# Kernel optimization log

Hardware: AMD Instinct MI355X
Metric: run time of the kernel (lower is better)

Reference implementation:

```python
import jax, jax.numpy as jnp
import numpy as np

Q_HEADS, KV_HEADS, DIMS = 16, 4, 1024
HEAD_DIM = DIMS // Q_HEADS          # 64
GROUPS = Q_HEADS // KV_HEADS        # 4


def rope(x):
    # x: [..., s, d]; base-10 thetas, positions start at 1 (per source RoPE)
    s, d = x.shape[-2], x.shape[-1]
    thetas = 10.0 ** (-jnp.arange(d // 2, dtype=jnp.float32))
    angles = jnp.arange(1, s + 1, dtype=jnp.float32)[:, None] * thetas  # [s, d/2]
    cos, sin = jnp.cos(angles), jnp.sin(angles)
    xr, xi = x[..., ::2], x[..., 1::2]
    outr = xr * cos - xi * sin
    outi = xr * sin + xi * cos
    return jnp.stack([outr, outi], axis=-1).reshape(x.shape)  # re-interleave


def setup_inputs() -> dict:
    key = jax.random.key(0)
    ks = jax.random.split(key, 5)
    b, s, in_dim = 4, 2048, 1024
    q = jax.random.normal(ks[0], (b, s, in_dim), dtype=jnp.float32)
    mask = jnp.tril(jnp.ones((s, s), dtype=jnp.float32))  # 1 = keep, 0 = masked
    sc = 1.0 / np.sqrt(in_dim)
    Wq = jax.random.normal(ks[1], (in_dim, Q_HEADS, HEAD_DIM), dtype=jnp.float32) * sc
    Wk = jax.random.normal(ks[2], (in_dim, KV_HEADS, HEAD_DIM), dtype=jnp.float32) * sc
    Wv = jax.random.normal(ks[3], (in_dim, KV_HEADS, HEAD_DIM), dtype=jnp.float32) * sc
    Wo = jax.random.normal(ks[4], (KV_HEADS * HEAD_DIM, in_dim), dtype=jnp.float32) * (1.0 / np.sqrt(KV_HEADS * HEAD_DIM))
    return {"q": q, "mask": mask, "Wq": Wq, "Wk": Wk, "Wv": Wv, "Wo": Wo}


def reference(q, mask, Wq, Wk, Wv, Wo):
    b, s, in_dim = q.shape
    # projections (DenseGeneral, no bias)
    qh = jnp.einsum('bsi,ihd->bshd', q, Wq)   # [b, s, 16, 64]
    kh = jnp.einsum('bsi,ihd->bshd', q, Wk)   # [b, s, 4, 64]  (kv = q)
    vh = jnp.einsum('bsi,ihd->bshd', q, Wv)
    # '... s (h g) d -> ... g h s d' with g=GROUPS
    qh = qh.reshape(b, s, KV_HEADS, GROUPS, HEAD_DIM).transpose(0, 3, 2, 1, 4)  # [b,g,h,s,d]
    kh = kh.transpose(0, 2, 1, 3)  # [b, h, s, d]
    vh = vh.transpose(0, 2, 1, 3)
    qh = rope(qh)
    kh = rope(kh)
    # NOTE: source einsum sums over group axis g
    scores = jnp.einsum('bghsd,bhad->bhsa', qh, kh)  # [b, h, s, s]
    scores = scores - (1.0 / mask - 1.0)             # mask==0 -> -inf
    attn = jax.nn.softmax(scores / jnp.float32(HEAD_DIM ** 0.5), axis=-1)
    out = jnp.einsum('bhsa,bhad->bhsd', attn, vh)    # [b, h, s, d]
    out = out.transpose(0, 2, 1, 3).reshape(b, s, KV_HEADS * HEAD_DIM)
    return out @ Wo  # [b, s, in_dim]
```

## Files before the change

### kernel.cpp

```cpp
#include <hip/hip_runtime.h>
#include <math.h>

#define BATCH 4
#define SEQ   2048
#define DIN   1024
#define KVH   4
#define HD    64
#define MTOT  (BATCH*SEQ)
#define NPROJ 768
#define PROJ_STRIDE (BATCH*KVH*SEQ*HD)
#define NCHUNK_TOT 80

typedef unsigned short ushort_t;
typedef __attribute__((ext_vector_type(8))) short short8;
typedef __attribute__((ext_vector_type(4))) float f32x4;

#define QSCALE (0.125f * 1.44269504088896340736f)

__device__ inline ushort_t f2bf(float x) {
    union { float f; unsigned int u; } v; v.f = x;
    unsigned int r = v.u + 0x7fffu + ((v.u >> 16) & 1u);
    return (ushort_t)(r >> 16);
}
__device__ inline ushort_t f2bf_trunc(float x) {
    return (ushort_t)(__float_as_uint(x) >> 16);
}

__device__ inline void load16_lds(const ushort_t* g, ushort_t* l) {
    __builtin_amdgcn_global_load_lds(
        (const __attribute__((address_space(1))) void*)g,
        (__attribute__((address_space(3))) void*)l, 16, 0, 0);
}

__global__ __launch_bounds__(256) void prep_kernel(
        const float* __restrict__ Wq, const float* __restrict__ Wk,
        const float* __restrict__ Wv, const float* __restrict__ Wo,
        const float* __restrict__ X,
        ushort_t* __restrict__ Wcat_t, ushort_t* __restrict__ Wo_t,
        float2* __restrict__ ctab, ushort_t* __restrict__ Y) {
    const int bx = blockIdx.x;
    const int tid = threadIdx.x;
    if (bx < 4096) {
        int idx = bx * 256 + tid;
        if (idx < NPROJ * DIN) {
            int n = idx >> 10, k = idx & 1023;
            float v;
            if (n < 256) {
                const float* p = Wq + (size_t)k * 1024 + (n >> 6) * 256 + (n & 63);
                v = p[0] + p[64] + p[128] + p[192];
            } else if (n < 512) {
                v = Wk[(size_t)k * 256 + (n - 256)];
            } else {
                v = Wv[(size_t)k * 256 + (n - 512)];
            }
            Wcat_t[idx] = f2bf(v);
        } else {
            int t = idx - NPROJ * DIN;
            int n = t >> 8, k = t & 255;
            Wo_t[t] = f2bf(Wo[(size_t)k * 1024 + n]);
        }
    } else if (bx < 4352) {
        int t = (bx - 4096) * 256 + tid;
        int j = t & 31, s = t >> 5;
        float ang = (float)(s + 1) * exp10f(-(float)j);
        float sn, cs;
        sincosf(ang, &sn, &cs);
        ctab[t] = make_float2(cs, sn);
    } else {
        int i = ((bx - 4352) * 256 + tid) * 4;
        float4 v = *(const float4*)&X[i];
        ushort4 o;
        o.x = f2bf(v.x); o.y = f2bf(v.y); o.z = f2bf(v.z); o.w = f2bf(v.w);
        *(ushort4*)&Y[i] = o;
    }
}

template<int OUT_MODE>
__global__ __launch_bounds__(256) void gemm_mfma_kernel(
        const ushort_t* __restrict__ A, const ushort_t* __restrict__ Bt,
        float* __restrict__ Y, ushort_t* __restrict__ Qbf,
        ushort_t* __restrict__ Kbf, ushort_t* __restrict__ Vt,
        const float2* __restrict__ ctab, int K, int N) {
    __shared__ __align__(16) ushort_t As[128 * 64];
    __shared__ __align__(16) ushort_t Bs[64 * 64];
    const int tid  = threadIdx.x;
    const int w    = tid >> 6, lane = tid & 63;
    const int m15  = lane & 15, quad = lane >> 4;
    const int wm   = (w >> 1) * 64, wn = (w & 1) * 32;
    const int m0   = blockIdx.y * 128, n0 = blockIdx.x * 64;
    const int r8   = lane >> 3;
    const int cs   = (((lane & 7) + r8) & 7) * 8;
    const int rotr = (m15 & 7) * 8;
    const int off0 = (quad * 8 + 64 - rotr) & 63;
    const int off1 = (32 + quad * 8 + 64 - rotr) & 63;

    f32x4 acc[4][2];
    #pragma unroll
    for (int i = 0; i < 4; ++i)
        #pragma unroll
        for (int j = 0; j < 2; ++j) acc[i][j] = (f32x4){0.f, 0.f, 0.f, 0.f};

    for (int k0 = 0; k0 < K; k0 += 64) {
        __syncthreads();
        #pragma unroll
        for (int p = 0; p < 4; ++p)
            load16_lds(A + (size_t)(m0 + w * 32 + p * 8 + r8) * K + k0 + cs,
                       As + (w * 32 + p * 8) * 64);
        #pragma unroll
        for (int p = 0; p < 2; ++p)
            load16_lds(Bt + (size_t)(n0 + w * 16 + p * 8 + r8) * K + k0 + cs,
                       Bs + (w * 16 + p * 8) * 64);
        __syncthreads();

        short8 af[4][2], bfm[2][2];
        #pragma unroll
        for (int i = 0; i < 4; ++i) {
            af[i][0] = *(const short8*)&As[(wm + i * 16 + m15) * 64 + off0];
            af[i][1] = *(const short8*)&As[(wm + i * 16 + m15) * 64 + off1];
        }
        #pragma unroll
        for (int j = 0; j < 2; ++j) {
            bfm[j][0] = *(const short8*)&Bs[(wn + j * 16 + m15) * 64 + off0];
            bfm[j][1] = *(const short8*)&Bs[(wn + j * 16 + m15) * 64 + off1];
        }
        #pragma unroll
        for (int i = 0; i < 4; ++i)
            #pragma unroll
            for (int j = 0; j < 2; ++j) {
                acc[i][j] = __builtin_amdgcn_mfma_f32_16x16x32_bf16(
                                af[i][0], bfm[j][0], acc[i][j], 0, 0, 0);
                acc[i][j] = __builtin_amdgcn_mfma_f32_16x16x32_bf16(
                                af[i][1], bfm[j][1], acc[i][j], 0, 0, 0);
            }
    }

    if (OUT_MODE == 0) {
        #pragma unroll
        for (int i = 0; i < 4; ++i)
            #pragma unroll
            for (int r = 0; r < 4; ++r) {
                size_t row = (size_t)(m0 + wm + i * 16 + quad * 4 + r);
                #pragma unroll
                for (int j = 0; j < 2; ++j)
                    Y[row * N + n0 + wn + j * 16 + m15] = acc[i][j][r];
            }
    } else {
        #pragma unroll
        for (int j = 0; j < 2; ++j) {
            int c = n0 + wn + j * 16 + m15;
            int proj = c >> 8, cc = c & 255;
            int hd = cc >> 6, d = cc & 63;
            if (proj < 2) {
                int jj = d >> 1;
                float sgn = (d & 1) ? 1.0f : -1.0f;
                float qs  = (proj == 0) ? QSCALE : 1.0f;
                ushort_t* dst = (proj ? Kbf : Qbf) + (size_t)hd * SEQ * HD + d;
                #pragma unroll
                for (int i = 0; i < 4; ++i)
                    #pragma unroll
                    for (int r = 0; r < 4; ++r) {
                        int m = m0 + wm + i * 16 + quad * 4 + r;
                        int b = m >> 11, s = m & (SEQ - 1);
                        float x = acc[i][j][r];
                        float p = __shfl_xor(x, 1);
                        float2 ct = ctab[s * 32 + jj];
                        float o = (x * ct.x + sgn * p * ct.y) * qs;
                        dst[(((size_t)b * KVH) * SEQ + s) * HD] = f2bf(o);
                    }
            } else {
                ushort_t* Vp = Vt + (((size_t)hd * HD) + d) * SEQ;
                #pragma unroll
                for (int i = 0; i < 4; ++i)
                    #pragma unroll
                    for (int r = 0; r < 4; ++r) {
                        int m = m0 + wm + i * 16 + quad * 4 + r;
                        int b = m >> 11, s = m & (SEQ - 1);
                        Vp[(size_t)b * KVH * HD * SEQ + s] = f2bf(acc[i][j][r]);
                    }
            }
        }
    }
}

__global__ __launch_bounds__(256) void attn_mfma_kernel(
        const ushort_t* __restrict__ Qbf, const ushort_t* __restrict__ Kbf,
        const ushort_t* __restrict__ Vtbf, float* __restrict__ pO,
        float* __restrict__ pL) {
    __shared__ __align__(16) ushort_t Ks[64][72];
    __shared__ __align__(16) ushort_t Vts[64][72];
    __shared__ __align__(16) ushort_t Ps[4][16][72];
    const int tid  = threadIdx.x;
    const int w    = tid >> 6, lane = tid & 63;
    const int m15  = lane & 15, quad = lane >> 4;
    const int bh   = blockIdx.y;
    const int f    = 79 - blockIdx.x;
    int qt, ch;
    if (f < 8)       { qt = f;                    ch = 0; }
    else if (f < 24) { qt = 8  + ((f - 8) >> 1);  ch = (f - 8) & 1; }
    else if (f < 48) { qt = 16 + (f - 24) / 3;    ch = (f - 24) % 3; }
    else             { qt = 24 + ((f - 48) >> 2); ch = (f - 48) & 3; }
    const int q0 = qt * 64;
    const int kt_beg = ch * 8;
    const int kt_end = min(kt_beg + 8, qt + 1);

    const ushort_t* Qb  = Qbf  + (size_t)bh * SEQ * HD;
    const ushort_t* Kb  = Kbf  + (size_t)bh * SEQ * HD;
    const ushort_t* Vtb = Vtbf + (size_t)bh * HD * SEQ;

    const int qrow = q0 + w * 16 + m15;
    short8 qf0 = *(const short8*)(Qb + (size_t)qrow * HD + quad * 8);
    short8 qf1 = *(const short8*)(Qb + (size_t)qrow * HD + 32 + quad * 8);

    f32x4 o[4];
    #pragma unroll
    for (int nt = 0; nt < 4; ++nt) o[nt] = (f32x4){0.f, 0.f, 0.f, 0.f};
    float lacc[4] = {0.f, 0.f, 0.f, 0.f};

    const int sc_ = tid & 7;
    const int sr_ = tid >> 3;

    short8 pk0, pk1, pv0, pv1;
    {
        const int k0 = kt_beg * 64;
        pk0 = *(const short8*)(Kb  + (size_t)(k0 + sr_) * HD + sc_ * 8);
        pk1 = *(const short8*)(Kb  + (size_t)(k0 + sr_ + 32) * HD + sc_ * 8);
        pv0 = *(const short8*)(Vtb + (size_t)sr_ * SEQ + k0 + sc_ * 8);
        pv1 = *(const short8*)(Vtb + (size_t)(sr_ + 32) * SEQ + k0 + sc_ * 8);
    }

    for (int kt = kt_beg; kt < kt_end; ++kt) {
        const int k0 = kt * 64;
        __syncthreads();
        *(short8*)&Ks[sr_][sc_*8]       = pk0;
        *(short8*)&Ks[sr_ + 32][sc_*8]  = pk1;
        *(short8*)&Vts[sr_][sc_*8]      = pv0;
        *(short8*)&Vts[sr_ + 32][sc_*8] = pv1;
        __syncthreads();

        if (kt + 1 < kt_end) {
            const int kn = k0 + 64;
            pk0 = *(const short8*)(Kb  + (size_t)(kn + sr_) * HD + sc_ * 8);
            pk1 = *(const short8*)(Kb  + (size_t)(kn + sr_ + 32) * HD + sc_ * 8);
            pv0 = *(const short8*)(Vtb + (size_t)sr_ * SEQ + kn + sc_ * 8);
            pv1 = *(const short8*)(Vtb + (size_t)(sr_ + 32) * SEQ + kn + sc_ * 8);
        }

        f32x4 sc4[4];
        #pragma unroll
        for (int nt = 0; nt < 4; ++nt) {
            f32x4 c = {0.f, 0.f, 0.f, 0.f};
            c = __builtin_amdgcn_mfma_f32_16x16x32_bf16(
                    qf0, *(const short8*)&Ks[nt*16 + m15][quad*8], c, 0, 0, 0);
            c = __builtin_amdgcn_mfma_f32_16x16x32_bf16(
                    qf1, *(const short8*)&Ks[nt*16 + m15][32 + quad*8], c, 0, 0, 0);
            sc4[nt] = c;
        }
        if (kt == qt) {
            #pragma unroll
            for (int nt = 0; nt < 4; ++nt) {
                int colg = k0 + nt*16 + m15;
                #pragma unroll
                for (int r = 0; r < 4; ++r) {
                    int rowg = q0 + w*16 + quad*4 + r;
                    if (colg > rowg) sc4[nt][r] = -INFINITY;
                }
            }
        }

        #pragma unroll
        for (int nt = 0; nt < 4; ++nt)
            #pragma unroll
            for (int r = 0; r < 4; ++r) {
                float e = exp2f(sc4[nt][r]);
                lacc[r] += e;
                Ps[w][quad*4 + r][nt*16 + m15] = f2bf_trunc(e);
            }

        short8 pa0 = *(const short8*)&Ps[w][m15][quad*8];
        short8 pa1 = *(const short8*)&Ps[w][m15][32 + quad*8];
        #pragma unroll
        for (int nt = 0; nt < 4; ++nt) {
            o[nt] = __builtin_amdgcn_mfma_f32_16x16x32_bf16(
                        pa0, *(const short8*)&Vts[nt*16 + m15][quad*8], o[nt], 0, 0, 0);
            o[nt] = __builtin_amdgcn_mfma_f32_16x16x32_bf16(
                        pa1, *(const short8*)&Vts[nt*16 + m15][32 + quad*8], o[nt], 0, 0, 0);
        }
    }

    const int blk = bh * NCHUNK_TOT + f;
    #pragma unroll
    for (int r = 0; r < 4; ++r) {
        float ls = lacc[r];
        ls += __shfl_xor(ls, 1);
        ls += __shfl_xor(ls, 2);
        ls += __shfl_xor(ls, 4);
        ls += __shfl_xor(ls, 8);
        int row = w * 16 + quad * 4 + r;
        if (m15 == 0) pL[(size_t)blk * 64 + row] = ls;
        #pragma unroll
        for (int nt = 0; nt < 4; ++nt)
            pO[(size_t)blk * 4096 + row * 64 + nt * 16 + m15] = o[nt][r];
    }
}

__device__ inline int flat_of(int qt, int ch) {
    if (qt < 8)  return qt;
    if (qt < 16) return 8 + (qt - 8) * 2 + ch;
    if (qt < 24) return 24 + (qt - 16) * 3 + ch;
    return 48 + (qt - 24) * 4 + ch;
}

__global__ __launch_bounds__(256) void combine_kernel(
        const float* __restrict__ pO, const float* __restrict__ pL,
        ushort_t* __restrict__ Out) {
    const int qt = blockIdx.x, bh = blockIdx.y;
    const int tid = threadIdx.x;
    const int row = tid >> 2;
    const int cb = (tid & 3) * 16;
    const int nch = (qt >> 3) + 1;
    float acc[16] = {};
    float lsum = 0.f;
    for (int c = 0; c < nch; ++c) {
        int blk = bh * NCHUNK_TOT + flat_of(qt, c);
        const float* po = pO + (size_t)blk * 4096 + row * 64 + cb;
        lsum += pL[(size_t)blk * 64 + row];
        #pragma unroll
        for (int j = 0; j < 4; ++j) {
            float4 v = *(const float4*)&po[j * 4];
            acc[j*4+0] += v.x; acc[j*4+1] += v.y;
            acc[j*4+2] += v.z; acc[j*4+3] += v.w;
        }
    }
    float inv = 1.0f / lsum;
    int b = bh >> 2, h = bh & 3;
    int s = qt * 64 + row;
    ushort_t tmp[16];
    #pragma unroll
    for (int j = 0; j < 16; ++j) tmp[j] = f2bf(acc[j] * inv);
    ushort_t* dst = Out + ((size_t)b * SEQ + s) * (KVH * HD) + h * HD + cb;
    *(uint4*)dst = ((uint4*)tmp)[0];
    *(uint4*)(dst + 8) = ((uint4*)tmp)[1];
}

extern "C" void kernel_launch(void* const* d_in, const int* in_sizes, int n_in,
                              void* d_out, int out_size, void* d_ws, size_t ws_size,
                              hipStream_t stream) {
    const float* q  = (const float*)d_in[0];
    const float* Wq = (const float*)d_in[2];
    const float* Wk = (const float*)d_in[3];
    const float* Wv = (const float*)d_in[4];
    const float* Wo = (const float*)d_in[5];
    float* out = (float*)d_out;

    char* base = (char*)d_ws;
    ushort_t* wcat_t  = (ushort_t*)(base);
    ushort_t* wo_t    = (ushort_t*)(base + 0x180000);
    float2*   ctab    = (float2*)(base + 0x200000);
    ushort_t* qin_bf  = (ushort_t*)(base + 0x280000);
    ushort_t* attn_bf = (ushort_t*)(base + 0x280000);
    float*    pO      = (float*)(base + 0x680000);
    float*    pL      = (float*)(base + 0x1A80000);
    ushort_t* q_bf    = (ushort_t*)(base + 0x1B00000);
    ushort_t* k_bf    = (ushort_t*)(base + 0x1F00000);
    ushort_t* vt_bf   = (ushort_t*)(base + 0x2300000);

    prep_kernel<<<12544, 256, 0, stream>>>(Wq, Wk, Wv, Wo, q,
                                           wcat_t, wo_t, ctab, qin_bf);

    dim3 gproj(NPROJ / 64, MTOT / 128);
    gemm_mfma_kernel<1><<<gproj, 256, 0, stream>>>(
        qin_bf, wcat_t, nullptr, q_bf, k_bf, vt_bf, ctab, DIN, NPROJ);

    dim3 gattn(NCHUNK_TOT, BATCH * KVH);
    attn_mfma_kernel<<<gattn, 256, 0, stream>>>(q_bf, k_bf, vt_bf, pO, pL);

    dim3 gcomb(SEQ / 64, BATCH * KVH);
    combine_kernel<<<gcomb, 256, 0, stream>>>(pO, pL, attn_bf);

    dim3 gout(DIN / 64, MTOT / 128);
    gemm_mfma_kernel<0><<<gout, 256, 0, stream>>>(
        attn_bf, wo_t, out, nullptr, nullptr, nullptr, nullptr, KVH * HD, DIN);
}
```

Baseline: 178.2 us.

## Register-prefetch next GEMM K tile and stagger K start per block row

Result: no change. 178.3 us (+0.0%).

```diff
diff --git a/kernel.cpp b/kernel.cpp
--- a/kernel.cpp
+++ b/kernel.cpp
@@ -24,12 +24,6 @@
 }
 __device__ inline ushort_t f2bf_trunc(float x) {
     return (ushort_t)(__float_as_uint(x) >> 16);
-}
-
-__device__ inline void load16_lds(const ushort_t* g, ushort_t* l) {
-    __builtin_amdgcn_global_load_lds(
-        (const __attribute__((address_space(1))) void*)g,
-        (__attribute__((address_space(3))) void*)l, 16, 0, 0);
 }
 
 __global__ __launch_bounds__(256) void prep_kernel(
@@ -89,28 +83,51 @@
     const int wm   = (w >> 1) * 64, wn = (w & 1) * 32;
     const int m0   = blockIdx.y * 128, n0 = blockIdx.x * 64;
     const int r8   = lane >> 3;
+    const int c8   = (lane & 7) * 8;
     const int cs   = (((lane & 7) + r8) & 7) * 8;
     const int rotr = (m15 & 7) * 8;
     const int off0 = (quad * 8 + 64 - rotr) & 63;
     const int off1 = (32 + quad * 8 + 64 - rotr) & 63;
 
+    const int niter = K >> 6;
+    const int kst   = blockIdx.y & (niter - 1);
+
     f32x4 acc[4][2];
     #pragma unroll
     for (int i = 0; i < 4; ++i)
         #pragma unroll
         for (int j = 0; j < 2; ++j) acc[i][j] = (f32x4){0.f, 0.f, 0.f, 0.f};
 
-    for (int k0 = 0; k0 < K; k0 += 64) {
+    short8 ra[4], rb[2];
+    {
+        const int k0 = kst * 64;
+        #pragma unroll
+        for (int p = 0; p < 4; ++p)
+            ra[p] = *(const short8*)(A + (size_t)(m0 + w * 32 + p * 8 + r8) * K + k0 + cs);
+        #pragma unroll
+        for (int p = 0; p < 2; ++p)
+            rb[p] = *(const short8*)(Bt + (size_t)(n0 + w * 16 + p * 8 + r8) * K + k0 + cs);
+    }
+
+    for (int it = 0; it < niter; ++it) {
         __syncthreads();
         #pragma unroll
         for (int p = 0; p < 4; ++p)
-            load16_lds(A + (size_t)(m0 + w * 32 + p * 8 + r8) * K + k0 + cs,
-                       As + (w * 32 + p * 8) * 64);
+            *(short8*)&As[(w * 32 + p * 8 + r8) * 64 + c8] = ra[p];
         #pragma unroll
         for (int p = 0; p < 2; ++p)
-            load16_lds(Bt + (size_t)(n0 + w * 16 + p * 8 + r8) * K + k0 + cs,
-                       Bs + (w * 16 + p * 8) * 64);
+            *(short8*)&Bs[(w * 16 + p * 8 + r8) * 64 + c8] = rb[p];
         __syncthreads();
+
+        if (it + 1 < niter) {
+            const int kn = ((kst + it + 1) & (niter - 1)) * 64;
+            #pragma unroll
+            for (int p = 0; p < 4; ++p)
+                ra[p] = *(const short8*)(A + (size_t)(m0 + w * 32 + p * 8 + r8) * K + kn + cs);
+            #pragma unroll
+            for (int p = 0; p < 2; ++p)
+                rb[p] = *(const short8*)(Bt + (size_t)(n0 + w * 16 + p * 8 + r8) * K + kn + cs);
+        }
 
         short8 af[4][2], bfm[2][2];
         #pragma unroll
```
